# Performance work log

Hardware: AMD Instinct MI355X
Metric: run time of the kernel (lower is better)

## Reference

```python
import jax, jax.numpy as jnp
import numpy as np

T, B, D, H = 256, 128, 128, 1024
MEL = 48           # preprocess.melodyRange
MELODY_COEFF = 0.5
FORGET_BIAS = 1.0  # TF BasicLSTMCell default


def setup_inputs() -> dict:
    key = jax.random.key(0)
    ks = jax.random.split(key, 8)
    s = 0.05
    return {
        "inSeq": jax.random.normal(ks[0], (T, B, D), dtype=jnp.float32),
        "targetSeq": jax.random.randint(ks[1], (T, B, 2), 0, MEL).astype(jnp.int64),
        "W1": jax.random.normal(ks[2], (D + H, 4 * H), dtype=jnp.float32) * s,
        "b1": jnp.zeros((4 * H,), dtype=jnp.float32),
        "W2": jax.random.normal(ks[3], (2 * H, 4 * H), dtype=jnp.float32) * s,
        "b2": jnp.zeros((4 * H,), dtype=jnp.float32),
        "outW": jax.random.normal(ks[4], (H, D), dtype=jnp.float32) * s,
        "outB": jnp.zeros((D,), dtype=jnp.float32),
    }


def _lstm_cell(x, c, h, W, b):
    # TF BasicLSTMCell: gates in (i, j, f, o) order, forget_bias added to f
    z = jnp.concatenate([x, h], axis=-1) @ W + b
    i, j, f, o = jnp.split(z, 4, axis=-1)
    c_new = c * jax.nn.sigmoid(f + FORGET_BIAS) + jax.nn.sigmoid(i) * jnp.tanh(j)
    h_new = jnp.tanh(c_new) * jax.nn.sigmoid(o)
    return c_new, h_new


def _forward(inSeq, targetSeq, W1, b1, W2, b2, outW, outB):
    dt = inSeq.dtype
    zero = jnp.zeros((B, H), dtype=dt)

    def step(carry, x):
        c1, h1, c2, h2 = carry
        c1, h1 = _lstm_cell(x, c1, h1, W1, b1)
        c2, h2 = _lstm_cell(h1, c2, h2, W2, b2)
        return (c1, h1, c2, h2), h2

    _, outputs = jax.lax.scan(step, (zero, zero, zero, zero), inSeq)  # [T,B,H]
    logits = outputs @ outW + outB                                    # [T,B,D]

    mel_logits = logits[..., :MEL]
    har_logits = logits[..., MEL:]

    # probs: per-timestep dual softmax, concatenated
    probs = jnp.concatenate(
        [jax.nn.softmax(mel_logits, axis=-1), jax.nn.softmax(har_logits, axis=-1)],
        axis=-1,
    )

    # dual sparse softmax cross-entropy
    mel_lp = jax.nn.log_softmax(mel_logits, axis=-1)
    har_lp = jax.nn.log_softmax(har_logits, axis=-1)
    mel_ce = -jnp.take_along_axis(mel_lp, targetSeq[..., 0:1], axis=-1)[..., 0]
    har_ce = -jnp.take_along_axis(har_lp, targetSeq[..., 1:2], axis=-1)[..., 0]
    losses = MELODY_COEFF * mel_ce + (1.0 - MELODY_COEFF) * har_ce
    loss = jnp.sum(losses) / T / B
    return probs, loss


def reference(inSeq, targetSeq, W1, b1, W2, b2, outW, outB):
    return _forward(inSeq, targetSeq, W1, b1, W2, b2, outW, outB)
```

## Files before the change

kernel.cpp:

```cpp
#include <hip/hip_runtime.h>
#include <cstdint>
#include <cstddef>

#define T_ 256
#define B_ 128
#define D_ 128
#define H_ 1024
#define K1_ 1152
#define K2_ 2048

typedef __bf16 bf16x8 __attribute__((ext_vector_type(8)));
typedef short s8 __attribute__((ext_vector_type(8)));
typedef float f32x4 __attribute__((ext_vector_type(4)));

__device__ __forceinline__ unsigned short f2bf(float f) {
  unsigned int u = __builtin_bit_cast(unsigned int, f);
  u += 0x7fff + ((u >> 16) & 1);
  return (unsigned short)(u >> 16);
}
__device__ __forceinline__ float sigm(float x) { return 1.f / (1.f + __expf(-x)); }
__device__ __forceinline__ float tanh_(float x) { return 1.f - 2.f / (__expf(2.f * x) + 1.f); }

__device__ __forceinline__ f32x4 mfma16(s8 a, s8 b, f32x4 c) {
  return __builtin_amdgcn_mfma_f32_16x16x32_bf16(
      __builtin_bit_cast(bf16x8, a), __builtin_bit_cast(bf16x8, b), c, 0, 0, 0);
}

__global__ void prep_misc(const float* __restrict__ inSeq,
                          const float* __restrict__ outW,
                          unsigned short* __restrict__ xbf,
                          unsigned short* __restrict__ outWp,
                          unsigned short* __restrict__ h1b,
                          unsigned short* __restrict__ h2all,
                          float* __restrict__ c1, float* __restrict__ c2,
                          float* __restrict__ loss)
{
  int i = blockIdx.x * 256 + threadIdx.x;
  if (i < T_ * B_ * D_) xbf[i] = f2bf(inSeq[i]);
  if (i < B_ * H_) {
    c1[i] = 0.f; c2[i] = 0.f;
    h1b[B_ * H_ + i] = 0;
    h2all[i] = 0;
  }
  if (i < H_ * D_) {
    int c = i >> 10, k = i & 1023;
    outWp[i] = f2bf(outW[(size_t)k * D_ + c]);
  }
  if (i == 0) loss[0] = 0.f;
}

__global__ void pack_w(const float* __restrict__ src, unsigned short* __restrict__ dst, int K)
{
  __shared__ float tile[64][65];
  int k0 = blockIdx.x * 64, j0 = blockIdx.y * 64, g = blockIdx.z;
  int tid = threadIdx.x;
#pragma unroll
  for (int e = 0; e < 16; ++e) {
    int li = e * 256 + tid;
    int kl = li >> 6, jl = li & 63;
    tile[kl][jl] = src[(size_t)(k0 + kl) * 4096 + g * 1024 + j0 + jl];
  }
  __syncthreads();
#pragma unroll
  for (int e = 0; e < 16; ++e) {
    int li = e * 256 + tid;
    int jl = li >> 6, kl = li & 63;
    dst[(size_t)((j0 + jl) * 4 + g) * K + k0 + kl] = f2bf(tile[kl][jl]);
  }
}

__global__ __launch_bounds__(256, 2) void phase_kernel(
    int p,
    const unsigned short* __restrict__ xbf,
    const unsigned short* __restrict__ W1p,
    const unsigned short* __restrict__ W2p,
    const float* __restrict__ b1,
    const float* __restrict__ b2,
    unsigned short* __restrict__ h1b,
    unsigned short* __restrict__ h2all,
    float* __restrict__ c1,
    float* __restrict__ c2)
{
  __shared__ float red[4][2048];
  const int bid = blockIdx.x;
  const bool isL2 = bid >= 256;
  if (!isL2 && p >= T_) return;
  if (isL2 && p == 0) return;
  const int jb = isL2 ? (bid - 256) : bid;
  const int mt = jb & 1, nt = jb >> 1;
  const int t = isL2 ? (p - 1) : p;
  const int r0 = mt * 64, c0 = nt * 32;
  const int tid = threadIdx.x;
  const int wid = tid >> 6, lane = tid & 63;
  const int quad = lane >> 4, l15 = lane & 15;
  const int kseg = quad * 8;

  const unsigned short* hsrc = h1b + (size_t)((p + 1) & 1) * (B_ * H_);

  f32x4 acc[4][2];
#pragma unroll
  for (int i = 0; i < 4; ++i)
#pragma unroll
    for (int j = 0; j < 2; ++j) acc[i][j] = (f32x4){0.f, 0.f, 0.f, 0.f};

  int arow[4], bcol[2];
#pragma unroll
  for (int i = 0; i < 4; ++i) arow[i] = r0 + i * 16 + l15;
#pragma unroll
  for (int j = 0; j < 2; ++j) bcol[j] = c0 + j * 16 + l15;

  if (!isL2) {
    const unsigned short* xt = xbf + (size_t)t * (B_ * D_);
    const int cpw = 9;
    const int kcbase = wid * cpw;
    s8 a[4], b[2], an[4], bn[2];
    auto LD = [&](int kc, s8* A, s8* Bv) {
      int kk = kc * 32 + kseg;
      if (kk < D_) {
#pragma unroll
        for (int i = 0; i < 4; ++i) A[i] = *(const s8*)(xt + (size_t)arow[i] * D_ + kk);
      } else {
#pragma unroll
        for (int i = 0; i < 4; ++i) A[i] = *(const s8*)(hsrc + (size_t)arow[i] * H_ + (kk - D_));
      }
#pragma unroll
      for (int j = 0; j < 2; ++j) Bv[j] = *(const s8*)(W1p + (size_t)bcol[j] * K1_ + kk);
    };
    LD(kcbase, a, b);
    for (int c = 0; c < cpw; ++c) {
      if (c + 1 < cpw) LD(kcbase + c + 1, an, bn);
#pragma unroll
      for (int i = 0; i < 4; ++i)
#pragma unroll
        for (int j = 0; j < 2; ++j) acc[i][j] = mfma16(a[i], b[j], acc[i][j]);
#pragma unroll
      for (int i = 0; i < 4; ++i) a[i] = an[i];
      b[0] = bn[0]; b[1] = bn[1];
    }
  } else {
    const unsigned short* h2prev = h2all + (size_t)t * (B_ * H_);
    const int cpw = 16;
    const int kcbase = wid * cpw;
    s8 a[4], b[2], an[4], bn[2];
    auto LD = [&](int kc, s8* A, s8* Bv) {
      int kk = kc * 32 + kseg;
      if (kk < H_) {
#pragma unroll
        for (int i = 0; i < 4; ++i) A[i] = *(const s8*)(hsrc + (size_t)arow[i] * H_ + kk);
      } else {
#pragma unroll
        for (int i = 0; i < 4; ++i) A[i] = *(const s8*)(h2prev + (size_t)arow[i] * H_ + (kk - H_));
      }
#pragma unroll
      for (int j = 0; j < 2; ++j) Bv[j] = *(const s8*)(W2p + (size_t)bcol[j] * K2_ + kk);
    };
    LD(kcbase, a, b);
    for (int c = 0; c < cpw; ++c) {
      if (c + 1 < cpw) LD(kcbase + c + 1, an, bn);
#pragma unroll
      for (int i = 0; i < 4; ++i)
#pragma unroll
        for (int j = 0; j < 2; ++j) acc[i][j] = mfma16(a[i], b[j], acc[i][j]);
#pragma unroll
      for (int i = 0; i < 4; ++i) a[i] = an[i];
      b[0] = bn[0]; b[1] = bn[1];
    }
  }

#pragma unroll
  for (int i = 0; i < 4; ++i)
#pragma unroll
    for (int j = 0; j < 2; ++j)
#pragma unroll
      for (int r = 0; r < 4; ++r)
        red[wid][(i * 16 + quad * 4 + r) * 32 + (j * 16 + l15)] = acc[i][j][r];
  __syncthreads();
#pragma unroll
  for (int it = 0; it < 8; ++it) {
    int e = it * 256 + tid;
    red[0][e] = red[0][e] + red[1][e] + red[2][e] + red[3][e];
  }
  __syncthreads();

  const float* bias = isL2 ? b2 : b1;
  float* cst = isL2 ? c2 : c1;
  unsigned short* hout = isL2 ? (h2all + (size_t)(t + 1) * (B_ * H_))
                              : (h1b + (size_t)(p & 1) * (B_ * H_));
#pragma unroll
  for (int it = 0; it < 2; ++it) {
    int s = it * 256 + tid;
    int row = s >> 3, u = s & 7;
    int jg = (c0 >> 2) + u;
    float zi = red[0][row * 32 + u * 4 + 0] + bias[0 * H_ + jg];
    float zj = red[0][row * 32 + u * 4 + 1] + bias[1 * H_ + jg];
    float zf = red[0][row * 32 + u * 4 + 2] + bias[2 * H_ + jg];
    float zo = red[0][row * 32 + u * 4 + 3] + bias[3 * H_ + jg];
    int rg = r0 + row;
    float co = cst[(size_t)rg * H_ + jg];
    float cn = co * sigm(zf + 1.0f) + sigm(zi) * tanh_(zj);
    float hn = tanh_(cn) * sigm(zo);
    cst[(size_t)rg * H_ + jg] = cn;
    hout[(size_t)rg * H_ + jg] = f2bf(hn);
  }
}

__global__ __launch_bounds__(256, 1) void proj_kernel(
    const unsigned short* __restrict__ h2flat,
    const unsigned short* __restrict__ outWp,
    const float* __restrict__ outB,
    const int* __restrict__ targets,
    float* __restrict__ out,
    float* __restrict__ loss)
{
  __shared__ float lg[128][129];
  __shared__ float red2[256];
  const int r0 = blockIdx.x * 128;
  const int tid = threadIdx.x;
  const int wid = tid >> 6, lane = tid & 63;
  const int quad = lane >> 4, l15 = lane & 15;
  const int wr = (wid & 1) * 64, wc = (wid >> 1) * 64;
  const int kseg = quad * 8;

  f32x4 acc[4][4];
#pragma unroll
  for (int i = 0; i < 4; ++i)
#pragma unroll
    for (int j = 0; j < 4; ++j) acc[i][j] = (f32x4){0.f, 0.f, 0.f, 0.f};

  int arow[4], bcolv[4];
#pragma unroll
  for (int i = 0; i < 4; ++i) arow[i] = r0 + wr + i * 16 + l15;
#pragma unroll
  for (int j = 0; j < 4; ++j) bcolv[j] = wc + j * 16 + l15;

  s8 a[4], b[4], an[4], bn[4];
  auto LD = [&](int kc, s8* A, s8* Bv) {
    int kk = kc * 32 + kseg;
#pragma unroll
    for (int i = 0; i < 4; ++i) A[i] = *(const s8*)(h2flat + (size_t)arow[i] * H_ + kk);
#pragma unroll
    for (int j = 0; j < 4; ++j) Bv[j] = *(const s8*)(outWp + (size_t)bcolv[j] * H_ + kk);
  };
  LD(0, a, b);
  for (int c = 0; c < 32; ++c) {
    if (c + 1 < 32) LD(c + 1, an, bn);
#pragma unroll
    for (int i = 0; i < 4; ++i)
#pragma unroll
      for (int j = 0; j < 4; ++j) acc[i][j] = mfma16(a[i], b[j], acc[i][j]);
#pragma unroll
    for (int i = 0; i < 4; ++i) a[i] = an[i];
#pragma unroll
    for (int j = 0; j < 4; ++j) b[j] = bn[j];
  }

#pragma unroll
  for (int i = 0; i < 4; ++i)
#pragma unroll
    for (int j = 0; j < 4; ++j)
#pragma unroll
      for (int r = 0; r < 4; ++r)
        lg[wr + i * 16 + quad * 4 + r][wc + j * 16 + l15] = acc[i][j][r] + outB[bcolv[j]];
  __syncthreads();

  const int row = tid >> 1, half = tid & 1;
  const int cbeg = half ? 48 : 0, cend = half ? 128 : 48;
  float m = -1e30f;
  for (int c = cbeg; c < cend; ++c) m = fmaxf(m, lg[row][c]);
  float s = 0.f;
  for (int c = cbeg; c < cend; ++c) s += __expf(lg[row][c] - m);
  float rinv = 1.f / s;
  float* orow = out + (size_t)(r0 + row) * D_;
  for (int c = cbeg; c < cend; ++c) orow[c] = __expf(lg[row][c] - m) * rinv;

  int tg = targets[(size_t)(r0 + row) * 2 + half];
  int tc = half ? (48 + tg) : tg;
  float ce = -(lg[row][tc] - m - logf(s));
  red2[tid] = 0.5f * ce;
  __syncthreads();
  for (int o = 128; o > 0; o >>= 1) {
    if (tid < o) red2[tid] += red2[tid + o];
    __syncthreads();
  }
  if (tid == 0) atomicAdd(loss, red2[0]);
}

__global__ void finalize_loss(const float* __restrict__ loss, float* __restrict__ out)
{
  out[(size_t)T_ * B_ * D_] = loss[0] * (1.f / (float)(T_ * B_));
}

extern "C" void kernel_launch(void* const* d_in, const int* in_sizes, int n_in,
                              void* d_out, int out_size, void* d_ws, size_t ws_size,
                              hipStream_t stream)
{
  const float* inSeq = (const float*)d_in[0];
  const int* targets = (const int*)d_in[1];
  const float* W1 = (const float*)d_in[2];
  const float* b1 = (const float*)d_in[3];
  const float* W2 = (const float*)d_in[4];
  const float* b2 = (const float*)d_in[5];
  const float* outW = (const float*)d_in[6];
  const float* outB = (const float*)d_in[7];
  float* out = (float*)d_out;

  char* w = (char*)d_ws;
  auto alloc = [&](size_t bytes) {
    char* r = w;
    w += (bytes + 255) & ~(size_t)255;
    return r;
  };
  unsigned short* W1p = (unsigned short*)alloc((size_t)4096 * K1_ * 2);
  unsigned short* W2p = (unsigned short*)alloc((size_t)4096 * K2_ * 2);
  unsigned short* xbf = (unsigned short*)alloc((size_t)T_ * B_ * D_ * 2);
  unsigned short* h1b = (unsigned short*)alloc((size_t)2 * B_ * H_ * 2);
  unsigned short* h2all = (unsigned short*)alloc((size_t)(T_ + 1) * B_ * H_ * 2);
  float* c1 = (float*)alloc((size_t)B_ * H_ * 4);
  float* c2 = (float*)alloc((size_t)B_ * H_ * 4);
  unsigned short* outWp = (unsigned short*)alloc((size_t)H_ * D_ * 2);
  float* loss = (float*)alloc(256);

  prep_misc<<<dim3((T_ * B_ * D_) / 256), dim3(256), 0, stream>>>(
      inSeq, outW, xbf, outWp, h1b, h2all, c1, c2, loss);
  pack_w<<<dim3(K1_ / 64, 16, 4), dim3(256), 0, stream>>>(W1, W1p, K1_);
  pack_w<<<dim3(K2_ / 64, 16, 4), dim3(256), 0, stream>>>(W2, W2p, K2_);

  for (int p = 0; p <= T_; ++p)
    phase_kernel<<<dim3(512), dim3(256), 0, stream>>>(
        p, xbf, W1p, W2p, b1, b2, h1b, h2all, c1, c2);

  proj_kernel<<<dim3(256), dim3(256), 0, stream>>>(
      h2all + (size_t)B_ * H_, outWp, outB, targets, out, loss);
  finalize_loss<<<dim3(1), dim3(1), 0, stream>>>(loss, out);
}
```

Baseline: 5.740 ms.

## Replace per-timestep kernel launches with a persistent kernel and grid barrier

The 257 per-phase launches become a single persistent kernel of 256 blocks with 512 threads. Inside each block, 3 waves compute the layer-1 tile and 5 waves compute the layer-2 tile for the same output slice, and blocks synchronise between phases with a global atomic counter barrier. This removes kernel launch and drain overhead on the sequential recurrence. In exchange it depends on all 256 blocks being co-resident, and it adds spin-wait barrier latency every step along with a less balanced split of K work across waves.

```diff
diff --git a/kernel.cpp b/kernel.cpp
--- a/kernel.cpp
+++ b/kernel.cpp
@@ -8,6 +8,7 @@
 #define H_ 1024
 #define K1_ 1152
 #define K2_ 2048
+#define NBLK 256
 
 typedef __bf16 bf16x8 __attribute__((ext_vector_type(8)));
 typedef short s8 __attribute__((ext_vector_type(8)));
@@ -33,7 +34,8 @@
                           unsigned short* __restrict__ h1b,
                           unsigned short* __restrict__ h2all,
                           float* __restrict__ c1, float* __restrict__ c2,
-                          float* __restrict__ loss)
+                          float* __restrict__ loss,
+                          unsigned* __restrict__ bar)
 {
   int i = blockIdx.x * 256 + threadIdx.x;
   if (i < T_ * B_ * D_) xbf[i] = f2bf(inSeq[i]);
@@ -46,7 +48,7 @@
     int c = i >> 10, k = i & 1023;
     outWp[i] = f2bf(outW[(size_t)k * D_ + c]);
   }
-  if (i == 0) loss[0] = 0.f;
+  if (i == 0) { loss[0] = 0.f; bar[0] = 0u; bar[1] = 0u; }
 }
 
 __global__ void pack_w(const float* __restrict__ src, unsigned short* __restrict__ dst, int K)
@@ -69,8 +71,7 @@
   }
 }
 
-__global__ __launch_bounds__(256, 2) void phase_kernel(
-    int p,
+__global__ __launch_bounds__(512, 2) void persist_kernel(
     const unsigned short* __restrict__ xbf,
     const unsigned short* __restrict__ W1p,
     const unsigned short* __restrict__ W2p,
@@ -79,29 +80,22 @@
     unsigned short* __restrict__ h1b,
     unsigned short* __restrict__ h2all,
     float* __restrict__ c1,
-    float* __restrict__ c2)
-{
-  __shared__ float red[4][2048];
+    float* __restrict__ c2,
+    unsigned* bar)
+{
+  __shared__ float red[8][2048];
   const int bid = blockIdx.x;
-  const bool isL2 = bid >= 256;
-  if (!isL2 && p >= T_) return;
-  if (isL2 && p == 0) return;
-  const int jb = isL2 ? (bid - 256) : bid;
-  const int mt = jb & 1, nt = jb >> 1;
-  const int t = isL2 ? (p - 1) : p;
-  const int r0 = mt * 64, c0 = nt * 32;
   const int tid = threadIdx.x;
-  const int wid = tid >> 6, lane = tid & 63;
+  const int wid = tid >> 6;
+  const int lane = tid & 63;
   const int quad = lane >> 4, l15 = lane & 15;
   const int kseg = quad * 8;
-
-  const unsigned short* hsrc = h1b + (size_t)((p + 1) & 1) * (B_ * H_);
-
-  f32x4 acc[4][2];
-#pragma unroll
-  for (int i = 0; i < 4; ++i)
-#pragma unroll
-    for (int j = 0; j < 2; ++j) acc[i][j] = (f32x4){0.f, 0.f, 0.f, 0.f};
+  const bool isL2 = wid >= 3;
+  const int htid = isL2 ? (tid - 192) : tid;
+  const int nthr = isL2 ? 320 : 192;
+  const int wv = isL2 ? (wid - 3) : wid;
+  const int mt = bid & 1, nt = bid >> 1;
+  const int r0 = mt * 64, c0 = nt * 32;
 
   int arow[4], bcol[2];
 #pragma unroll
@@ -109,98 +103,137 @@
 #pragma unroll
   for (int j = 0; j < 2; ++j) bcol[j] = c0 + j * 16 + l15;
 
-  if (!isL2) {
-    const unsigned short* xt = xbf + (size_t)t * (B_ * D_);
-    const int cpw = 9;
-    const int kcbase = wid * cpw;
-    s8 a[4], b[2], an[4], bn[2];
-    auto LD = [&](int kc, s8* A, s8* Bv) {
-      int kk = kc * 32 + kseg;
-      if (kk < D_) {
-#pragma unroll
-        for (int i = 0; i < 4; ++i) A[i] = *(const s8*)(xt + (size_t)arow[i] * D_ + kk);
+  unsigned* bar_cnt = bar;
+  unsigned* bar_rel = bar + 1;
+
+  for (int p = 0; p <= T_; ++p) {
+    const bool active = isL2 ? (p >= 1) : (p < T_);
+    const unsigned short* hsrc = h1b + (size_t)((p + 1) & 1) * (B_ * H_);
+
+    if (active) {
+      f32x4 acc[4][2];
+#pragma unroll
+      for (int i = 0; i < 4; ++i)
+#pragma unroll
+        for (int j = 0; j < 2; ++j) acc[i][j] = (f32x4){0.f, 0.f, 0.f, 0.f};
+
+      if (!isL2) {
+        const unsigned short* xt = xbf + (size_t)p * (B_ * D_);
+        const int kcbase = wv * 12;
+        s8 a[4], b[2], an[4], bn[2];
+        auto LD = [&](int kc, s8* A, s8* Bv) {
+          int kk = kc * 32 + kseg;
+          if (kk < D_) {
+#pragma unroll
+            for (int i = 0; i < 4; ++i) A[i] = *(const s8*)(xt + (size_t)arow[i] * D_ + kk);
+          } else {
+#pragma unroll
+            for (int i = 0; i < 4; ++i) A[i] = *(const s8*)(hsrc + (size_t)arow[i] * H_ + (kk - D_));
+          }
+#pragma unroll
+          for (int j = 0; j < 2; ++j) Bv[j] = *(const s8*)(W1p + (size_t)bcol[j] * K1_ + kk);
+        };
+        LD(kcbase, a, b);
+        for (int c = 0; c < 12; ++c) {
+          if (c + 1 < 12) LD(kcbase + c + 1, an, bn);
+#pragma unroll
+          for (int i = 0; i < 4; ++i)
+#pragma unroll
+            for (int j = 0; j < 2; ++j) acc[i][j] = mfma16(a[i], b[j], acc[i][j]);
+#pragma unroll
+          for (int i = 0; i < 4; ++i) a[i] = an[i];
+          b[0] = bn[0]; b[1] = bn[1];
+        }
       } else {
-#pragma unroll
-        for (int i = 0; i < 4; ++i) A[i] = *(const s8*)(hsrc + (size_t)arow[i] * H_ + (kk - D_));
+        const unsigned short* h2prev = h2all + (size_t)(p - 1) * (B_ * H_);
+        const int kcbase = wv * 13;
+        const int cnt = (kcbase + 13 <= 64) ? 13 : (64 - kcbase);
+        s8 a[4], b[2], an[4], bn[2];
+        auto LD = [&](int kc, s8* A, s8* Bv) {
+          int kk = kc * 32 + kseg;
+          if (kk < H_) {
+#pragma unroll
+            for (int i = 0; i < 4; ++i) A[i] = *(const s8*)(hsrc + (size_t)arow[i] * H_ + kk);
+          } else {
+#pragma unroll
+            for (int i = 0; i < 4; ++i) A[i] = *(const s8*)(h2prev + (size_t)arow[i] * H_ + (kk - H_));
+          }
+#pragma unroll
+          for (int j = 0; j < 2; ++j) Bv[j] = *(const s8*)(W2p + (size_t)bcol[j] * K2_ + kk);
+        };
+        LD(kcbase, a, b);
+        for (int c = 0; c < cnt; ++c) {
+          if (c + 1 < cnt) LD(kcbase + c + 1, an, bn);
+#pragma unroll
+          for (int i = 0; i < 4; ++i)
+#pragma unroll
+            for (int j = 0; j < 2; ++j) acc[i][j] = mfma16(a[i], b[j], acc[i][j]);
+#pragma unroll
+          for (int i = 0; i < 4; ++i) a[i] = an[i];
+          b[0] = bn[0]; b[1] = bn[1];
+        }
       }
-#pragma unroll
-      for (int j = 0; j < 2; ++j) Bv[j] = *(const s8*)(W1p + (size_t)bcol[j] * K1_ + kk);
-    };
-    LD(kcbase, a, b);
-    for (int c = 0; c < cpw; ++c) {
-      if (c + 1 < cpw) LD(kcbase + c + 1, an, bn);
+
 #pragma unroll
       for (int i = 0; i < 4; ++i)
 #pragma unroll
-        for (int j = 0; j < 2; ++j) acc[i][j] = mfma16(a[i], b[j], acc[i][j]);
-#pragma unroll
-      for (int i = 0; i < 4; ++i) a[i] = an[i];
-      b[0] = bn[0]; b[1] = bn[1];
+        for (int j = 0; j < 2; ++j)
+#pragma unroll
+          for (int r = 0; r < 4; ++r)
+            red[wid][(i * 16 + quad * 4 + r) * 32 + (j * 16 + l15)] = acc[i][j][r];
     }
-  } else {
-    const unsigned short* h2prev = h2all + (size_t)t * (B_ * H_);
-    const int cpw = 16;
-    const int kcbase = wid * cpw;
-    s8 a[4], b[2], an[4], bn[2];
-    auto LD = [&](int kc, s8* A, s8* Bv) {
-      int kk = kc * 32 + kseg;
-      if (kk < H_) {
-#pragma unroll
-        for (int i = 0; i < 4; ++i) A[i] = *(const s8*)(hsrc + (size_t)arow[i] * H_ + kk);
+    __syncthreads();
+
+    if (active) {
+      if (!isL2) {
+        for (int e = htid; e < 2048; e += 192)
+          red[0][e] = red[0][e] + red[1][e] + red[2][e];
       } else {
-#pragma unroll
-        for (int i = 0; i < 4; ++i) A[i] = *(const s8*)(h2prev + (size_t)arow[i] * H_ + (kk - H_));
+        for (int e = htid; e < 2048; e += 320)
+          red[3][e] = red[3][e] + red[4][e] + red[5][e] + red[6][e] + red[7][e];
       }
-#pragma unroll
-      for (int j = 0; j < 2; ++j) Bv[j] = *(const s8*)(W2p + (size_t)bcol[j] * K2_ + kk);
-    };
-    LD(kcbase, a, b);
-    for (int c = 0; c < cpw; ++c) {
-      if (c + 1 < cpw) LD(kcbase + c + 1, an, bn);
-#pragma unroll
-      for (int i = 0; i < 4; ++i)
-#pragma unroll
-        for (int j = 0; j < 2; ++j) acc[i][j] = mfma16(a[i], b[j], acc[i][j]);
-#pragma unroll
-      for (int i = 0; i < 4; ++i) a[i] = an[i];
-      b[0] = bn[0]; b[1] = bn[1];
     }
-  }
-
-#pragma unroll
-  for (int i = 0; i < 4; ++i)
-#pragma unroll
-    for (int j = 0; j < 2; ++j)
-#pragma unroll
-      for (int r = 0; r < 4; ++r)
-        red[wid][(i * 16 + quad * 4 + r) * 32 + (j * 16 + l15)] = acc[i][j][r];
-  __syncthreads();
-#pragma unroll
-  for (int it = 0; it < 8; ++it) {
-    int e = it * 256 + tid;
-    red[0][e] = red[0][e] + red[1][e] + red[2][e] + red[3][e];
-  }
-  __syncthreads();
-
-  const float* bias = isL2 ? b2 : b1;
-  float* cst = isL2 ? c2 : c1;
-  unsigned short* hout = isL2 ? (h2all + (size_t)(t + 1) * (B_ * H_))
-                              : (h1b + (size_t)(p & 1) * (B_ * H_));
-#pragma unroll
-  for (int it = 0; it < 2; ++it) {
-    int s = it * 256 + tid;
-    int row = s >> 3, u = s & 7;
-    int jg = (c0 >> 2) + u;
-    float zi = red[0][row * 32 + u * 4 + 0] + bias[0 * H_ + jg];
-    float zj = red[0][row * 32 + u * 4 + 1] + bias[1 * H_ + jg];
-    float zf = red[0][row * 32 + u * 4 + 2] + bias[2 * H_ + jg];
-    float zo = red[0][row * 32 + u * 4 + 3] + bias[3 * H_ + jg];
-    int rg = r0 + row;
-    float co = cst[(size_t)rg * H_ + jg];
-    float cn = co * sigm(zf + 1.0f) + sigm(zi) * tanh_(zj);
-    float hn = tanh_(cn) * sigm(zo);
-    cst[(size_t)rg * H_ + jg] = cn;
-    hout[(size_t)rg * H_ + jg] = f2bf(hn);
+    __syncthreads();
+
+    if (active) {
+      const float* bias = isL2 ? b2 : b1;
+      float* cst = isL2 ? c2 : c1;
+      unsigned short* hout = isL2 ? (h2all + (size_t)p * (B_ * H_))
+                                  : (h1b + (size_t)(p & 1) * (B_ * H_));
+      const float* rr = red[isL2 ? 3 : 0];
+      for (int s = htid; s < 512; s += nthr) {
+        int row = s >> 3, u = s & 7;
+        int jg = (c0 >> 2) + u;
+        float zi = rr[row * 32 + u * 4 + 0] + bias[0 * H_ + jg];
+        float zj = rr[row * 32 + u * 4 + 1] + bias[1 * H_ + jg];
+        float zf = rr[row * 32 + u * 4 + 2] + bias[2 * H_ + jg];
+        float zo = rr[row * 32 + u * 4 + 3] + bias[3 * H_ + jg];
+        int rg = r0 + row;
+        float co = cst[(size_t)rg * H_ + jg];
+        float cn = co * sigm(zf + 1.0f) + sigm(zi) * tanh_(zj);
+        float hn = tanh_(cn) * sigm(zo);
+        cst[(size_t)rg * H_ + jg] = cn;
+        hout[(size_t)rg * H_ + jg] = f2bf(hn);
+      }
+    }
+    __syncthreads();
+
+    if (tid == 0) {
+      __threadfence();
+      unsigned target = (unsigned)(p + 1) * NBLK;
+      unsigned a = __hip_atomic_fetch_add(bar_cnt, 1u, __ATOMIC_ACQ_REL,
+                                          __HIP_MEMORY_SCOPE_AGENT) + 1u;
+      if (a == target) {
+        __hip_atomic_store(bar_rel, target, __ATOMIC_RELEASE,
+                           __HIP_MEMORY_SCOPE_AGENT);
+      } else {
+        while (__hip_atomic_load(bar_rel, __ATOMIC_ACQUIRE,
+                                 __HIP_MEMORY_SCOPE_AGENT) < target)
+          __builtin_amdgcn_s_sleep(1);
+      }
+      __threadfence();
+    }
+    __syncthreads();
   }
 }
 
@@ -319,15 +352,15 @@
   float* c2 = (float*)alloc((size_t)B_ * H_ * 4);
   unsigned short* outWp = (unsigned short*)alloc((size_t)H_ * D_ * 2);
   float* loss = (float*)alloc(256);
+  unsigned* bar = (unsigned*)alloc(256);
 
   prep_misc<<<dim3((T_ * B_ * D_) / 256), dim3(256), 0, stream>>>(
-      inSeq, outW, xbf, outWp, h1b, h2all, c1, c2, loss);
+      inSeq, outW, xbf, outWp, h1b, h2all, c1, c2, loss, bar);
   pack_w<<<dim3(K1_ / 64, 16, 4), dim3(256), 0, stream>>>(W1, W1p, K1_);
   pack_w<<<dim3(K2_ / 64, 16, 4), dim3(256), 0, stream>>>(W2, W2p, K2_);
 
-  for (int p = 0; p <= T_; ++p)
-    phase_kernel<<<dim3(512), dim3(256), 0, stream>>>(
-        p, xbf, W1p, W2p, b1, b2, h1b, h2all, c1, c2);
+  persist_kernel<<<dim3(NBLK), dim3(512), 0, stream>>>(
+      xbf, W1p, W2p, b1, b2, h1b, h2all, c1, c2, bar);
 
   proj_kernel<<<dim3(256), dim3(256), 0, stream>>>(
       h2all + (size_t)B_ * H_, outWp, outB, targets, out, loss);
```

Measured after the change: 12.08 ms. +110.5%, slower.
